# Kernel optimization log

Hardware: AMD Instinct MI355X
Metric: run time of the kernel (lower is better)

## Reference

```python
import jax, jax.numpy as jnp
import numpy as np

EPS = 1e-6


def setup_inputs() -> dict:
    key = jax.random.key(0)
    kH, kE1, kE2, kM, kW = jax.random.split(key, 5)
    B, N, D, E, L = 16, 2048, 64, 32768, 2
    H = jax.random.normal(kH, (B, N, D), dtype=jnp.float32)
    src = jax.random.randint(kE1, (B, 1, E), 0, N)
    dst = jax.random.randint(kE2, (B, 1, E), 0, N)
    edge_index = jnp.concatenate([src, dst], axis=1)  # [B, 2, E]
    m = jax.random.uniform(kM, (B, E), dtype=jnp.float32)
    W = jax.random.normal(kW, (L, D, D), dtype=jnp.float32) * (1.0 / np.sqrt(D))
    return {"H": H, "edge_index": edge_index, "m": m, "W": W}


def reference(H, edge_index, m, W):
    # H: [B, N, D]; edge_index: [B, 2, E] int; m: [B, E]; W: [L, D, D]
    B, N, _ = H.shape
    L = W.shape[0]
    bidx = jnp.arange(B)[:, None]          # [B, 1] broadcasts against [B, E]
    src = edge_index[:, 0, :]
    dst = edge_index[:, 1, :]
    A = jnp.zeros((B, N, N), dtype=H.dtype)
    # batched scatter: A[b, src, dst] = m; A[b, dst, src] = m (symmetric fill)
    A = A.at[bidx, src, dst].set(m)
    A = A.at[bidx, dst, src].set(m)
    A = A + jnp.eye(N, dtype=H.dtype)[None]  # add self loops
    deg = jnp.clip(A.sum(axis=-1), EPS)       # [B, N]
    dis = deg ** -0.5
    A_norm = dis[:, :, None] * A * dis[:, None, :]  # D^-1/2 A D^-1/2
    X = H
    for l in range(L):
        X = jnp.einsum('bnm,bmd->bnd', A_norm, X)
        X = jnp.einsum('bnd,ed->bne', X, W[l])  # Linear: X @ W^T
        if l < L - 1:
            X = jax.nn.gelu(X, approximate=False)  # torch GELU (exact erf); dropout in eval mode
    return X
```

## Files before the change

kernel.cpp:

```cpp
#include <hip/hip_runtime.h>
#include <stdint.h>
#include <math.h>

#define BATCH 16
#define NNODE 2048
#define DDIM  64
#define NEDGE 32768
#define SEG   32
#define SLOTS 128
#define NROWS (BATCH*NNODE)
#define RPB   128

__global__ void k_build(const int* __restrict__ ei, const float* __restrict__ m,
                        uint32_t* __restrict__ cnt4, uint2* __restrict__ entries) {
    __shared__ uint32_t cntS[RPB];
    __shared__ uint32_t keyS[RPB][SEG];
    __shared__ float    valS[RPB][SEG];

    int b  = blockIdx.x & 15;
    int gh = blockIdx.x >> 4;
    int r0 = (gh >> 2) * RPB;
    int q  = gh & 3;
    int t  = threadIdx.x;

    if (t < RPB) cntS[t] = 0u;
    __syncthreads();

    const int*   eb = ei + (size_t)b * 2 * NEDGE;
    const float* mb = m  + (size_t)b * NEDGE;
    int e0 = q * (NEDGE / 4);

    for (int i = 0; i < 4; ++i) {
        int e4 = e0 + i * 2048 + t * 4;
        int4   s4 = *(const int4*)(eb + e4);
        int4   d4 = *(const int4*)(eb + NEDGE + e4);
        float4 m4 = *(const float4*)(mb + e4);
        #pragma unroll
        for (int j = 0; j < 4; ++j) {
            int   src = j == 0 ? s4.x : j == 1 ? s4.y : j == 2 ? s4.z : s4.w;
            int   dst = j == 0 ? d4.x : j == 1 ? d4.y : j == 2 ? d4.z : d4.w;
            float mv  = j == 0 ? m4.x : j == 1 ? m4.y : j == 2 ? m4.z : m4.w;
            int e  = e4 + j;
            int rs = src - r0;
            if ((unsigned)rs < RPB) {
                uint32_t p = atomicAdd(&cntS[rs], 1u);
                if (p < SEG) { keyS[rs][p] = (uint32_t)dst | ((uint32_t)e << 11); valS[rs][p] = mv; }
            }
            int rd = dst - r0;
            if ((unsigned)rd < RPB) {
                uint32_t p = atomicAdd(&cntS[rd], 1u);
                if (p < SEG) { keyS[rd][p] = (uint32_t)src | ((uint32_t)(NEDGE + e) << 11); valS[rd][p] = mv; }
            }
        }
    }
    __syncthreads();

    int lane = t & 63;
    int wid  = t >> 6;
    int pos  = lane & 31;
    int sub  = lane >> 5;
    for (int rr = 0; rr < 8; ++rr) {
        int r  = wid * 16 + rr * 2 + sub;
        int rg = b * NNODE + r0 + r;
        int k  = (int)min(cntS[r], (uint32_t)SEG);
        size_t base = (size_t)rg * SLOTS + q * SEG;
        if (pos < k)
            entries[base + pos] = make_uint2(keyS[r][pos], __float_as_uint(valS[r][pos]));
        if (pos == 0) cnt4[rg * 4 + q] = (uint32_t)k;
    }
}

__global__ void k_dedupe(const uint32_t* __restrict__ cnt4, uint2* __restrict__ entries,
                         uint32_t* __restrict__ cnt_fin,
                         float* __restrict__ dis, float* __restrict__ self) {
    __shared__ uint32_t tbl[4][NNODE];
    int b    = blockIdx.x & 15;
    int wv   = threadIdx.x >> 6;
    int w    = b * NNODE + (blockIdx.x >> 4) * 4 + wv;
    int lane = threadIdx.x & 63;
    uint32_t* T = tbl[wv];
    uint4 kq = ((const uint4*)cnt4)[w];
    int k0 = (int)kq.x, k1 = (int)kq.y, k2 = (int)kq.z, k3 = (int)kq.w;
    size_t base = (size_t)w * SLOTS;
    int pos = lane & 31;
    int klo = (lane < 32) ? k0 : k1;
    int khi = (lane < 32) ? k2 : k3;

    uint32_t key0 = 0u, key1 = 0u;
    float v0 = 0.f, v1 = 0.f;
    bool a0 = pos < klo;
    bool a1 = pos < khi;
    if (a0) { uint2 kv = entries[base + lane];      key0 = kv.x; v0 = __uint_as_float(kv.y); }
    if (a1) { uint2 kv = entries[base + 64 + lane]; key1 = kv.x; v1 = __uint_as_float(kv.y); }
    uint32_t c0 = key0 & 2047u, p0 = key0 >> 11;
    uint32_t c1 = key1 & 2047u, p1 = key1 >> 11;

    if (a0) T[c0] = 0u;
    if (a1) T[c1] = 0u;
    if (a0) atomicMax(&T[c0], p0);
    if (a1) atomicMax(&T[c1], p1);
    if (a0) a0 = (T[c0] == p0);
    if (a1) a1 = (T[c1] == p1);

    float sum = (a0 ? v0 : 0.f) + (a1 ? v1 : 0.f);
    for (int off = 32; off; off >>= 1) sum += __shfl_xor(sum, off, 64);
    float deg = fmaxf(1.0f + sum, 1e-6f);
    if (lane == 0) {
        float di = 1.0f / sqrtf(deg);
        dis[w]  = di;
        self[w] = di * di;
    }

    unsigned long long m0 = __ballot(a0);
    unsigned long long m1 = __ballot(a1);
    unsigned long long below = (1ull << lane) - 1ull;
    int n0 = __popcll(m0);
    if (a0) entries[base + __popcll(m0 & below)]      = make_uint2(key0, __float_as_uint(v0));
    if (a1) entries[base + n0 + __popcll(m1 & below)] = make_uint2(key1, __float_as_uint(v1));
    if (lane == 0) cnt_fin[w] = (uint32_t)(n0 + __popcll(m1));
}

__global__ void k_layer(const float* __restrict__ Xin, const float* __restrict__ W,
                        float* __restrict__ Xout,
                        const uint32_t* __restrict__ cnt_fin, const uint2* __restrict__ entries,
                        const float* __restrict__ dis, const float* __restrict__ self,
                        int dogelu) {
    __shared__ float WT[64 * 65];
    int Lb = blockIdx.x;
    int b  = Lb & 15;
    int rb = Lb >> 4;
    int t  = threadIdx.x;

    #pragma unroll
    for (int i = 0; i < 16; ++i) {
        int idx = i * 256 + t;
        WT[(idx & 63) * 65 + (idx >> 6)] = W[idx];
    }
    __syncthreads();

    int lane = t & 63;
    int wid  = t >> 6;
    const float* Xb   = Xin + (size_t)b * NNODE * DDIM;
    const char*  Xc   = (const char*)Xb + lane * 4;
    const float* disB = dis + (b << 11);

    int row0 = rb * 8 + wid * 2;
    int rg0  = b * NNODE + row0;

    uint32_t offAr[2], wAur[2], offBr[2], wBur[2];
    int      kkr[2];
    float    idr[2];
    #pragma unroll
    for (int rr = 0; rr < 2; ++rr) {
        int rg = rg0 + rr;
        int k  = (int)cnt_fin[rg];
        kkr[rr] = k;
        size_t base = (size_t)rg * SLOTS;
        uint32_t kA = 0u, vA = 0u, kB = 0u, vB = 0u;
        if (lane < k)      { uint2 kv = entries[base + lane];      kA = kv.x; vA = kv.y; }
        if (lane + 64 < k) { uint2 kv = entries[base + 64 + lane]; kB = kv.x; vB = kv.y; }
        float dr = disB[row0 + rr];
        int   colA = (int)(kA & 2047u);
        offAr[rr] = (uint32_t)colA << 8;
        wAur[rr]  = __float_as_uint(__uint_as_float(vA) * dr * disB[colA]);
        int   colB = (int)(kB & 2047u);
        offBr[rr] = (uint32_t)colB << 8;
        wBur[rr]  = __float_as_uint(__uint_as_float(vB) * dr * disB[colB]);
        idr[rr]   = self[rg] * Xb[(size_t)(row0 + rr) * DDIM + lane];
    }

    float accv[2];
    #pragma unroll
    for (int rr = 0; rr < 2; ++rr) {
        int k = kkr[rr];
        uint32_t offA = offAr[rr], wAu = wAur[rr];
        uint32_t offB = offBr[rr], wBu = wBur[rr];

        float acc0 = idr[rr];
        float acc1 = 0.f, acc2 = 0.f, acc3 = 0.f;

        int k0 = k < 64 ? k : 64;
        int e = 0;
        for (; e + 16 <= k0; e += 16) {
            float xv0, xv1, xv2, xv3, xv4, xv5, xv6, xv7;
            float xv8, xv9, xva, xvb, xvc, xvd, xve, xvf;
            float w0, w1, w2, w3, w4, w5, w6, w7;
            float w8, w9, wa, wb, wc, wd, we, wf;
            #define G(idx, X, Wv) { \
                uint32_t o = __builtin_amdgcn_readlane(offA, e + idx); \
                Wv = __uint_as_float(__builtin_amdgcn_readlane(wAu, e + idx)); \
                X = *(const float*)(Xc + o); }
            G(0, xv0, w0)  G(1, xv1, w1)  G(2, xv2, w2)  G(3, xv3, w3)
            G(4, xv4, w4)  G(5, xv5, w5)  G(6, xv6, w6)  G(7, xv7, w7)
            G(8, xv8, w8)  G(9, xv9, w9)  G(10, xva, wa) G(11, xvb, wb)
            G(12, xvc, wc) G(13, xvd, wd) G(14, xve, we) G(15, xvf, wf)
            #undef G
            acc0 = fmaf(w0, xv0, acc0); acc1 = fmaf(w1, xv1, acc1);
            acc2 = fmaf(w2, xv2, acc2); acc3 = fmaf(w3, xv3, acc3);
            acc0 = fmaf(w4, xv4, acc0); acc1 = fmaf(w5, xv5, acc1);
            acc2 = fmaf(w6, xv6, acc2); acc3 = fmaf(w7, xv7, acc3);
            acc0 = fmaf(w8, xv8, acc0); acc1 = fmaf(w9, xv9, acc1);
            acc2 = fmaf(wa, xva, acc2); acc3 = fmaf(wb, xvb, acc3);
            acc0 = fmaf(wc, xvc, acc0); acc1 = fmaf(wd, xvd, acc1);
            acc2 = fmaf(we, xve, acc2); acc3 = fmaf(wf, xvf, acc3);
        }
        for (; e + 4 <= k0; e += 4) {
            uint32_t o0 = __builtin_amdgcn_readlane(offA, e);
            uint32_t o1 = __builtin_amdgcn_readlane(offA, e + 1);
            uint32_t o2 = __builtin_amdgcn_readlane(offA, e + 2);
            uint32_t o3 = __builtin_amdgcn_readlane(offA, e + 3);
            float w0 = __uint_as_float(__builtin_amdgcn_readlane(wAu, e));
            float w1 = __uint_as_float(__builtin_amdgcn_readlane(wAu, e + 1));
            float w2 = __uint_as_float(__builtin_amdgcn_readlane(wAu, e + 2));
            float w3 = __uint_as_float(__builtin_amdgcn_readlane(wAu, e + 3));
            acc0 = fmaf(w0, *(const float*)(Xc + o0), acc0);
            acc1 = fmaf(w1, *(const float*)(Xc + o1), acc1);
            acc2 = fmaf(w2, *(const float*)(Xc + o2), acc2);
            acc3 = fmaf(w3, *(const float*)(Xc + o3), acc3);
        }
        for (; e < k0; ++e) {
            uint32_t o = __builtin_amdgcn_readlane(offA, e);
            float wv = __uint_as_float(__builtin_amdgcn_readlane(wAu, e));
            acc0 = fmaf(wv, *(const float*)(Xc + o), acc0);
        }
        for (e = 64; e < k; ++e) {
            uint32_t o = __builtin_amdgcn_readlane(offB, e - 64);
            float wv = __uint_as_float(__builtin_amdgcn_readlane(wBu, e - 64));
            acc1 = fmaf(wv, *(const float*)(Xc + o), acc1);
        }
        accv[rr] = (acc0 + acc1) + (acc2 + acc3);
    }

    uint32_t sa = __float_as_uint(accv[0]);
    uint32_t sb = __float_as_uint(accv[1]);
    float ya0 = 0.f, ya1 = 0.f, ya2 = 0.f, ya3 = 0.f;
    float yb0 = 0.f, yb1 = 0.f, yb2 = 0.f, yb3 = 0.f;
    #pragma unroll
    for (int d = 0; d < 64; d += 4) {
        float wt0 = WT[(d + 0) * 65 + lane];
        float wt1 = WT[(d + 1) * 65 + lane];
        float wt2 = WT[(d + 2) * 65 + lane];
        float wt3 = WT[(d + 3) * 65 + lane];
        ya0 = fmaf(__uint_as_float(__builtin_amdgcn_readlane(sa, d + 0)), wt0, ya0);
        ya1 = fmaf(__uint_as_float(__builtin_amdgcn_readlane(sa, d + 1)), wt1, ya1);
        ya2 = fmaf(__uint_as_float(__builtin_amdgcn_readlane(sa, d + 2)), wt2, ya2);
        ya3 = fmaf(__uint_as_float(__builtin_amdgcn_readlane(sa, d + 3)), wt3, ya3);
        yb0 = fmaf(__uint_as_float(__builtin_amdgcn_readlane(sb, d + 0)), wt0, yb0);
        yb1 = fmaf(__uint_as_float(__builtin_amdgcn_readlane(sb, d + 1)), wt1, yb1);
        yb2 = fmaf(__uint_as_float(__builtin_amdgcn_readlane(sb, d + 2)), wt2, yb2);
        yb3 = fmaf(__uint_as_float(__builtin_amdgcn_readlane(sb, d + 3)), wt3, yb3);
    }
    float ya = (ya0 + ya1) + (ya2 + ya3);
    float yb = (yb0 + yb1) + (yb2 + yb3);
    if (dogelu) {
        ya = 0.5f * ya * (1.0f + erff(ya * 0.70710678118654752440f));
        yb = 0.5f * yb * (1.0f + erff(yb * 0.70710678118654752440f));
    }
    Xout[((size_t)b * NNODE + row0)     * DDIM + lane] = ya;
    Xout[((size_t)b * NNODE + row0 + 1) * DDIM + lane] = yb;
}

extern "C" void kernel_launch(void* const* d_in, const int* in_sizes, int n_in,
                              void* d_out, int out_size, void* d_ws, size_t ws_size,
                              hipStream_t stream) {
    const float* H  = (const float*)d_in[0];
    const int*   ei = (const int*)d_in[1];
    const float* m  = (const float*)d_in[2];
    const float* W  = (const float*)d_in[3];
    float* out = (float*)d_out;

    char* ws = (char*)d_ws;
    uint32_t* cnt4    = (uint32_t*)ws;
    uint32_t* cnt_fin = (uint32_t*)(ws + (512 << 10));
    float*    dis     = (float*)(ws + (640 << 10));
    float*    self    = (float*)(ws + (768 << 10));
    uint2*    entries = (uint2*)(ws + (896 << 10));
    float*    X2      = (float*)(ws + (896 << 10) + (size_t)NROWS * SLOTS * 8);

    k_build <<<BATCH * (NNODE / RPB) * 4, 512, 0, stream>>>(ei, m, cnt4, entries);
    k_dedupe<<<NROWS / 4, 256, 0, stream>>>(cnt4, entries, cnt_fin, dis, self);
    k_layer <<<4096, 256, 0, stream>>>(H,  W,        X2,  cnt_fin, entries, dis, self, 1);
    k_layer <<<4096, 256, 0, stream>>>(X2, W + 4096, out, cnt_fin, entries, dis, self, 0);
}
```

Baseline: 145.9 us.

## Gather two neighbor rows per wave using half-wave float2 loads in SpMM

For rows with at most 64 neighbors, the sparse aggregation now splits the wave into two halves that each handle a different neighbor and load float2 (two features per lane), so each gather instruction covers two edges. Neighbor offsets and weights are distributed with ds_bpermute instead of scalar readlane. The half-wave partial sums are then combined with a cross-half shuffle and re-spread back to one feature per lane. This halves the number of gather iterations but adds LDS permute traffic and a final reduction, and rows with more than 64 neighbors keep the old path.

```diff
diff --git a/kernel.cpp b/kernel.cpp
--- a/kernel.cpp
+++ b/kernel.cpp
@@ -142,14 +142,16 @@
     int wid  = t >> 6;
     const float* Xb   = Xin + (size_t)b * NNODE * DDIM;
     const char*  Xc   = (const char*)Xb + lane * 4;
+    const char*  XcPK = (const char*)Xb + (lane & 31) * 8;
     const float* disB = dis + (b << 11);
 
     int row0 = rb * 8 + wid * 2;
     int rg0  = b * NNODE + row0;
+    uint32_t bsel = (uint32_t)(lane & 32) >> 3;
 
     uint32_t offAr[2], wAur[2], offBr[2], wBur[2];
     int      kkr[2];
-    float    idr[2];
+    float    selfS[2];
     #pragma unroll
     for (int rr = 0; rr < 2; ++rr) {
         int rg = rg0 + rr;
@@ -166,69 +168,84 @@
         int   colB = (int)(kB & 2047u);
         offBr[rr] = (uint32_t)colB << 8;
         wBur[rr]  = __float_as_uint(__uint_as_float(vB) * dr * disB[colB]);
-        idr[rr]   = self[rg] * Xb[(size_t)(row0 + rr) * DDIM + lane];
+        selfS[rr] = self[rg];
     }
 
     float accv[2];
     #pragma unroll
     for (int rr = 0; rr < 2; ++rr) {
         int k = kkr[rr];
+        int row = row0 + rr;
         uint32_t offA = offAr[rr], wAu = wAur[rr];
-        uint32_t offB = offBr[rr], wBu = wBur[rr];
-
-        float acc0 = idr[rr];
-        float acc1 = 0.f, acc2 = 0.f, acc3 = 0.f;
-
-        int k0 = k < 64 ? k : 64;
-        int e = 0;
-        for (; e + 16 <= k0; e += 16) {
-            float xv0, xv1, xv2, xv3, xv4, xv5, xv6, xv7;
-            float xv8, xv9, xva, xvb, xvc, xvd, xve, xvf;
-            float w0, w1, w2, w3, w4, w5, w6, w7;
-            float w8, w9, wa, wb, wc, wd, we, wf;
-            #define G(idx, X, Wv) { \
-                uint32_t o = __builtin_amdgcn_readlane(offA, e + idx); \
-                Wv = __uint_as_float(__builtin_amdgcn_readlane(wAu, e + idx)); \
-                X = *(const float*)(Xc + o); }
-            G(0, xv0, w0)  G(1, xv1, w1)  G(2, xv2, w2)  G(3, xv3, w3)
-            G(4, xv4, w4)  G(5, xv5, w5)  G(6, xv6, w6)  G(7, xv7, w7)
-            G(8, xv8, w8)  G(9, xv9, w9)  G(10, xva, wa) G(11, xvb, wb)
-            G(12, xvc, wc) G(13, xvd, wd) G(14, xve, we) G(15, xvf, wf)
-            #undef G
-            acc0 = fmaf(w0, xv0, acc0); acc1 = fmaf(w1, xv1, acc1);
-            acc2 = fmaf(w2, xv2, acc2); acc3 = fmaf(w3, xv3, acc3);
-            acc0 = fmaf(w4, xv4, acc0); acc1 = fmaf(w5, xv5, acc1);
-            acc2 = fmaf(w6, xv6, acc2); acc3 = fmaf(w7, xv7, acc3);
-            acc0 = fmaf(w8, xv8, acc0); acc1 = fmaf(w9, xv9, acc1);
-            acc2 = fmaf(wa, xva, acc2); acc3 = fmaf(wb, xvb, acc3);
-            acc0 = fmaf(wc, xvc, acc0); acc1 = fmaf(wd, xvd, acc1);
-            acc2 = fmaf(we, xve, acc2); acc3 = fmaf(wf, xvf, acc3);
+
+        if (k <= 64) {
+            float2 xid = *(const float2*)((const char*)Xb + (uint32_t)row * 256 + (lane & 31) * 8);
+            float idw = (lane < 32) ? selfS[rr] : 0.f;
+            float al0 = idw * xid.x, ah0 = idw * xid.y;
+            float al1 = 0.f, ah1 = 0.f, al2 = 0.f, ah2 = 0.f, al3 = 0.f, ah3 = 0.f;
+
+            int npair = (k + 1) >> 1;
+            int p = 0;
+            for (; p + 8 <= npair; p += 8) {
+                uint32_t o0, o1, o2, o3, o4, o5, o6, o7;
+                float w0, w1, w2, w3, w4, w5, w6, w7;
+                float2 x0, x1, x2, x3, x4, x5, x6, x7;
+                #define GP(i, O, WW, XV) { \
+                    O  = (uint32_t)__builtin_amdgcn_ds_bpermute((int)(bsel + 8u * (uint32_t)(p + i)), (int)offA); \
+                    WW = __uint_as_float((uint32_t)__builtin_amdgcn_ds_bpermute((int)(bsel + 8u * (uint32_t)(p + i)), (int)wAu)); \
+                    XV = *(const float2*)(XcPK + O); }
+                GP(0, o0, w0, x0) GP(1, o1, w1, x1) GP(2, o2, w2, x2) GP(3, o3, w3, x3)
+                GP(4, o4, w4, x4) GP(5, o5, w5, x5) GP(6, o6, w6, x6) GP(7, o7, w7, x7)
+                #undef GP
+                al0 = fmaf(w0, x0.x, al0); ah0 = fmaf(w0, x0.y, ah0);
+                al1 = fmaf(w1, x1.x, al1); ah1 = fmaf(w1, x1.y, ah1);
+                al2 = fmaf(w2, x2.x, al2); ah2 = fmaf(w2, x2.y, ah2);
+                al3 = fmaf(w3, x3.x, al3); ah3 = fmaf(w3, x3.y, ah3);
+                al0 = fmaf(w4, x4.x, al0); ah0 = fmaf(w4, x4.y, ah0);
+                al1 = fmaf(w5, x5.x, al1); ah1 = fmaf(w5, x5.y, ah1);
+                al2 = fmaf(w6, x6.x, al2); ah2 = fmaf(w6, x6.y, ah2);
+                al3 = fmaf(w7, x7.x, al3); ah3 = fmaf(w7, x7.y, ah3);
+            }
+            for (; p < npair; ++p) {
+                uint32_t o = (uint32_t)__builtin_amdgcn_ds_bpermute((int)(bsel + 8u * (uint32_t)p), (int)offA);
+                float    w = __uint_as_float((uint32_t)__builtin_amdgcn_ds_bpermute((int)(bsel + 8u * (uint32_t)p), (int)wAu));
+                float2   x = *(const float2*)(XcPK + o);
+                al0 = fmaf(w, x.x, al0); ah0 = fmaf(w, x.y, ah0);
+            }
+
+            float slo = (al0 + al1) + (al2 + al3);
+            float shi = (ah0 + ah1) + (ah2 + ah3);
+            slo += __shfl_xor(slo, 32, 64);
+            shi += __shfl_xor(shi, 32, 64);
+            uint32_t lg = (uint32_t)__builtin_amdgcn_ds_bpermute((lane >> 1) << 2, (int)__float_as_uint(slo));
+            uint32_t hg = (uint32_t)__builtin_amdgcn_ds_bpermute((lane >> 1) << 2, (int)__float_as_uint(shi));
+            accv[rr] = __uint_as_float((lane & 1) ? hg : lg);
+        } else {
+            uint32_t offB = offBr[rr], wBu = wBur[rr];
+            float acc0 = selfS[rr] * Xb[(size_t)row * DDIM + lane];
+            float acc1 = 0.f, acc2 = 0.f, acc3 = 0.f;
+            int e = 0;
+            for (; e + 4 <= 64; e += 4) {
+                uint32_t o0 = __builtin_amdgcn_readlane(offA, e);
+                uint32_t o1 = __builtin_amdgcn_readlane(offA, e + 1);
+                uint32_t o2 = __builtin_amdgcn_readlane(offA, e + 2);
+                uint32_t o3 = __builtin_amdgcn_readlane(offA, e + 3);
+                float w0 = __uint_as_float(__builtin_amdgcn_readlane(wAu, e));
+                float w1 = __uint_as_float(__builtin_amdgcn_readlane(wAu, e + 1));
+                float w2 = __uint_as_float(__builtin_amdgcn_readlane(wAu, e + 2));
+                float w3 = __uint_as_float(__builtin_amdgcn_readlane(wAu, e + 3));
+                acc0 = fmaf(w0, *(const float*)(Xc + o0), acc0);
+                acc1 = fmaf(w1, *(const float*)(Xc + o1), acc1);
+                acc2 = fmaf(w2, *(const float*)(Xc + o2), acc2);
+                acc3 = fmaf(w3, *(const float*)(Xc + o3), acc3);
+            }
+            for (e = 64; e < k; ++e) {
+                uint32_t o = __builtin_amdgcn_readlane(offB, e - 64);
+                float wv = __uint_as_float(__builtin_amdgcn_readlane(wBu, e - 64));
+                acc1 = fmaf(wv, *(const float*)(Xc + o), acc1);
+            }
+            accv[rr] = (acc0 + acc1) + (acc2 + acc3);
         }
-        for (; e + 4 <= k0; e += 4) {
-            uint32_t o0 = __builtin_amdgcn_readlane(offA, e);
-            uint32_t o1 = __builtin_amdgcn_readlane(offA, e + 1);
-            uint32_t o2 = __builtin_amdgcn_readlane(offA, e + 2);
-            uint32_t o3 = __builtin_amdgcn_readlane(offA, e + 3);
-            float w0 = __uint_as_float(__builtin_amdgcn_readlane(wAu, e));
-            float w1 = __uint_as_float(__builtin_amdgcn_readlane(wAu, e + 1));
-            float w2 = __uint_as_float(__builtin_amdgcn_readlane(wAu, e + 2));
-            float w3 = __uint_as_float(__builtin_amdgcn_readlane(wAu, e + 3));
-            acc0 = fmaf(w0, *(const float*)(Xc + o0), acc0);
-            acc1 = fmaf(w1, *(const float*)(Xc + o1), acc1);
-            acc2 = fmaf(w2, *(const float*)(Xc + o2), acc2);
-            acc3 = fmaf(w3, *(const float*)(Xc + o3), acc3);
-        }
-        for (; e < k0; ++e) {
-            uint32_t o = __builtin_amdgcn_readlane(offA, e);
-            float wv = __uint_as_float(__builtin_amdgcn_readlane(wAu, e));
-            acc0 = fmaf(wv, *(const float*)(Xc + o), acc0);
-        }
-        for (e = 64; e < k; ++e) {
-            uint32_t o = __builtin_amdgcn_readlane(offB, e - 64);
-            float wv = __uint_as_float(__builtin_amdgcn_readlane(wBu, e - 64));
-            acc1 = fmaf(wv, *(const float*)(Xc + o), acc1);
-        }
-        accv[rr] = (acc0 + acc1) + (acc2 + acc3);
     }
 
     uint32_t sa = __float_as_uint(accv[0]);
```

After: 150.1 us. +2.9%, slower.
